# Performance work log

Hardware: AMD Instinct MI355X
Metric: run time of the kernel (lower is better)

The kernel has to match this reference:

```python
import jax, jax.numpy as jnp
import numpy as np

B, CIN, COUT, K, H, W = 8, 512, 512, 3, 64, 64
SCALE = 1.0 / np.sqrt(CIN * K * K).astype(np.float32)  # conv.scale
LRELU_SCALE = 1.4142135623730951  # sqrt(2), FusedLeakyReLU scale


def setup_inputs() -> dict:
    key = jax.random.key(0)
    ks = jax.random.split(key, 6)
    return {
        "x": jax.random.normal(ks[0], (B, CIN, H, W), jnp.float32),
        "style": jax.random.normal(ks[1], (B, CIN), jnp.float32),
        "noise": jax.random.normal(ks[2], (1, 1, H, W), jnp.float32),
        "weight": jax.random.normal(ks[3], (COUT, CIN, K, K), jnp.float32),
        "bias": jnp.zeros((COUT,), jnp.float32),
        "noise_strength": jax.random.uniform(ks[4], (1,), jnp.float32),
    }


def reference(x, style, noise, weight, bias, noise_strength):
    # Modulate: scale * weight * style  -> [B, Cout, Cin, K, K]
    w = SCALE * weight[None] * style[:, None, :, None, None]
    # Demodulate per (batch, out_channel)
    demod = jax.lax.rsqrt(jnp.sum(w * w, axis=(2, 3, 4)) + 1e-8)
    w = w * demod[:, :, None, None, None]
    # Per-sample conv (grouped-conv trick in torch) via vmap over batch
    pad = K // 2
    def conv_one(xi, wi):  # xi: [Cin,H,W], wi: [Cout,Cin,K,K]
        return jax.lax.conv_general_dilated(
            xi[None], wi, window_strides=(1, 1),
            padding=[(pad, pad), (pad, pad)],
            dimension_numbers=("NCHW", "OIHW", "NCHW"))[0]
    out = jax.vmap(conv_one)(x, w)  # [B, Cout, H, W]
    # NoiseInjection: out + strength * noise (noise broadcast over B, C)
    out = out + noise_strength[0] * noise
    # FusedLeakyReLU: leaky_relu(out + bias, 0.2) * sqrt(2)
    y = out + bias[None, :, None, None]
    return jnp.where(y >= 0, y, 0.2 * y) * LRELU_SCALE
```

## Files before the change

kernel.cpp:

```cpp
#include <hip/hip_runtime.h>
#include <hip/hip_bf16.h>

typedef __attribute__((ext_vector_type(8))) short s16x8;
typedef __attribute__((ext_vector_type(4))) float f32x4;

#define MOD_SCALE 0.014731391274719739f

__device__ __forceinline__ void gload_lds16(const void* g, void* l) {
    __builtin_amdgcn_global_load_lds(
        (const __attribute__((address_space(1))) unsigned int*)g,
        (__attribute__((address_space(3))) unsigned int*)l, 16, 0, 0);
}

__global__ __launch_bounds__(256) void k_border(__hip_bfloat16* __restrict__ xs) {
    const int idx = blockIdx.x * 256 + threadIdx.x;
    const int b = idx / 16640;
    const int r2 = idx - b * 16640;
    const int pair = r2 >> 6;
    const int ciq = r2 & 63;
    int pr, pc;
    if (pair < 66)       { pr = 0;          pc = pair; }
    else if (pair < 132) { pr = 65;         pc = pair - 66; }
    else if (pair < 196) { pr = pair - 131; pc = 0; }
    else                 { pr = pair - 195; pc = 65; }
    uint4* d = (uint4*)(xs + (((size_t)b * 66 + pr) * 66 + pc) * 512) + ciq;
    *d = make_uint4(0u, 0u, 0u, 0u);
}

__global__ __launch_bounds__(256) void k_xprep(const float* __restrict__ x,
                                               const float* __restrict__ style,
                                               __hip_bfloat16* __restrict__ xs) {
    const int cig = blockIdx.x, h = blockIdx.y, b = blockIdx.z;
    const int ci0 = cig * 128;
    __shared__ __align__(16) __hip_bfloat16 tile[64][130];
    const int t = threadIdx.x;
    const int wl = t & 63, cl4 = t >> 6;
    for (int r = 0; r < 32; ++r) {
        int c = r * 4 + cl4;
        float v = x[(((size_t)b * 512 + ci0 + c) * 64 + h) * 64 + wl];
        float s = style[b * 512 + ci0 + c];
        tile[wl][c] = __float2bfloat16(v * s * MOD_SCALE);
    }
    __syncthreads();
    const int w4 = t >> 6;
    const int cp = (t & 63) * 2;
    for (int r = 0; r < 16; ++r) {
        int w = r * 4 + w4;
        unsigned v = *(const unsigned*)(&tile[w][cp]);
        *(unsigned*)(&xs[(((size_t)b * 66 + h + 1) * 66 + (w + 1)) * 512 +
                         ci0 + cp]) = v;
    }
}

__global__ __launch_bounds__(256) void k_wprep(const float* __restrict__ w,
                                               __hip_bfloat16* __restrict__ wb) {
    __shared__ float lds[2304];
    const int t = threadIdx.x;
    const int p0 = blockIdx.x * 256;
    const float* src = w + (size_t)p0 * 9;
#pragma unroll
    for (int k = 0; k < 9; ++k) lds[k * 256 + t] = src[k * 256 + t];
    __syncthreads();
#pragma unroll
    for (int tap = 0; tap < 9; ++tap)
        wb[(size_t)tap * 262144 + p0 + t] = __float2bfloat16(lds[t * 9 + tap]);
}

__global__ __launch_bounds__(256) void k_demod(const float* __restrict__ w,
                                               const float* __restrict__ style,
                                               float* __restrict__ dem) {
    const int co = blockIdx.x;
    const int t = threadIdx.x;
    float accb[8] = {0.f, 0.f, 0.f, 0.f, 0.f, 0.f, 0.f, 0.f};
    for (int ci = t; ci < 512; ci += 256) {
        const float* wp = w + ((size_t)co * 512 + ci) * 9;
        float ws = 0.f;
#pragma unroll
        for (int k = 0; k < 9; ++k) { float v = wp[k]; ws += v * v; }
#pragma unroll
        for (int bb = 0; bb < 8; ++bb) {
            float s = style[bb * 512 + ci];
            accb[bb] += s * s * ws;
        }
    }
    __shared__ float red[256];
    const float S2 = MOD_SCALE * MOD_SCALE;
    for (int bb = 0; bb < 8; ++bb) {
        red[t] = accb[bb];
        __syncthreads();
        for (int off = 128; off > 0; off >>= 1) {
            if (t < off) red[t] += red[t + off];
            __syncthreads();
        }
        if (t == 0) dem[bb * 512 + co] = rsqrtf(S2 * red[0] + 1e-8f);
        __syncthreads();
    }
}

__global__ __launch_bounds__(256, 3) void k_conv(
    const __hip_bfloat16* __restrict__ xs,
    const __hip_bfloat16* __restrict__ wb,
    const float* __restrict__ demod,
    const float* __restrict__ noise,
    const float* __restrict__ bias,
    const float* __restrict__ nstr,
    float* __restrict__ out) {
    __shared__ __align__(16) char Xl[264 * 64];
    __shared__ __align__(16) char Wl[384 * 64];

    const int t = threadIdx.x;
    const int bi = blockIdx.x;
    const int co0 = (bi & 3) * 128;
    const int h0 = ((bi >> 2) & 31) * 2;
    const int b = bi >> 7;
    const int lane = t & 63;
    const int wv = t >> 6;
    const int wm = wv & 1, wn = wv >> 1;
    const int q = lane >> 4, ln = lane & 15;

    f32x4 acc[4][4];
#pragma unroll
    for (int i = 0; i < 4; ++i)
#pragma unroll
        for (int j = 0; j < 4; ++j) acc[i][j] = (f32x4){0.f, 0.f, 0.f, 0.f};

    const char* xsb = (const char*)xs + (size_t)b * 66 * 66 * 1024;
    const char* xsrc[4];
#pragma unroll
    for (int i = 0; i < 4; ++i) {
        int g = i * 256 + t;
        int e = g >> 2, s = g & 3;
        int r = e / 66, c = e - r * 66;
        int gc = s ^ (e & 3);
        xsrc[i] = xsb + (size_t)((h0 + r) * 66 + c) * 1024 + gc * 16;
    }
    const char* xsrct = xsb;
    {
        int e = 256 + (t >> 2), s = t & 3;
        int c = e - 198;
        int gc = s ^ (e & 3);
        xsrct = xsb + (size_t)((h0 + 3) * 66 + c) * 1024 + gc * 16;
    }
    const char* wsrc[6];
#pragma unroll
    for (int i = 0; i < 6; ++i) {
        int g = i * 256 + t;
        int e = g >> 2, s = g & 3;
        int rr = e >> 7, co = e & 127;
        int gc = s ^ (co & 3);
        wsrc[i] = (const char*)wb +
                  ((size_t)rr * 262144 + (size_t)(co0 + co) * 512) * 2 + gc * 16;
    }
    char* ldsXw = Xl + (wv << 10);
    char* ldsWw = Wl + (wv << 10);

    for (int cb = 0; cb < 16; ++cb) {
        const int cboff = cb * 64;
        __syncthreads();
#pragma unroll
        for (int i = 0; i < 4; ++i)
            gload_lds16(xsrc[i] + cboff, ldsXw + i * 4096);
        if (t < 32) gload_lds16(xsrct + cboff, Xl + 16384);
#pragma unroll
        for (int i = 0; i < 6; ++i)
            gload_lds16(wsrc[i] + cboff, ldsWw + i * 4096);
        __syncthreads();

        for (int dh = 0; dh < 3; ++dh) {
            if (dh) {
                __syncthreads();
#pragma unroll
                for (int i = 0; i < 6; ++i)
                    gload_lds16(wsrc[i] + dh * 1572864 + cboff, ldsWw + i * 4096);
                __syncthreads();
            }
            const int xrow = dh + wn;
#pragma unroll
            for (int dw = 0; dw < 3; ++dw) {
                s16x8 af[4], bfr[4];
                const char* abase =
                    Wl + (dw * 128 + wm * 64 + ln) * 64 + ((q ^ (ln & 3)) << 4);
#pragma unroll
                for (int mi = 0; mi < 4; ++mi)
                    af[mi] = *(const s16x8*)(abase + mi * 1024);
                const int ecol = xrow * 66 + dw + ln;
                const char* bbase = Xl + ecol * 64 + ((q ^ (ecol & 3)) << 4);
#pragma unroll
                for (int ni = 0; ni < 4; ++ni)
                    bfr[ni] = *(const s16x8*)(bbase + ni * 1024);
#pragma unroll
                for (int mi = 0; mi < 4; ++mi)
#pragma unroll
                    for (int ni = 0; ni < 4; ++ni)
                        acc[mi][ni] = __builtin_amdgcn_mfma_f32_16x16x32_bf16(
                            af[mi], bfr[ni], acc[mi][ni], 0, 0, 0);
            }
        }
    }

    const float nsv = nstr[0];
    const int h = h0 + wn;
    const float LR = 1.4142135623730951f;
#pragma unroll
    for (int mi = 0; mi < 4; ++mi) {
        float dm[4], bs[4];
#pragma unroll
        for (int r = 0; r < 4; ++r) {
            int co = co0 + wm * 64 + mi * 16 + q * 4 + r;
            dm[r] = demod[b * 512 + co];
            bs[r] = bias[co];
        }
#pragma unroll
        for (int ni = 0; ni < 4; ++ni) {
            int w = ni * 16 + ln;
            float nz = nsv * noise[h * 64 + w];
#pragma unroll
            for (int r = 0; r < 4; ++r) {
                int co = co0 + wm * 64 + mi * 16 + q * 4 + r;
                float v = acc[mi][ni][r] * dm[r] + nz + bs[r];
                v = (v >= 0.f ? v : 0.2f * v) * LR;
                out[(((size_t)b * 512 + co) * 64 + h) * 64 + w] = v;
            }
        }
    }
}

extern "C" void kernel_launch(void* const* d_in, const int* in_sizes, int n_in,
                              void* d_out, int out_size, void* d_ws, size_t ws_size,
                              hipStream_t stream) {
    const float* x      = (const float*)d_in[0];
    const float* style  = (const float*)d_in[1];
    const float* noise  = (const float*)d_in[2];
    const float* weight = (const float*)d_in[3];
    const float* bias   = (const float*)d_in[4];
    const float* nstr   = (const float*)d_in[5];
    float* out = (float*)d_out;

    char* ws = (char*)d_ws;
    __hip_bfloat16* xs = (__hip_bfloat16*)ws;
    __hip_bfloat16* wb = (__hip_bfloat16*)(ws + 35684352);
    float* demod = (float*)(ws + 35684352 + 4718592);

    k_border<<<520, 256, 0, stream>>>(xs);
    k_xprep<<<dim3(4, 64, 8), 256, 0, stream>>>(x, style, xs);
    k_wprep<<<1024, 256, 0, stream>>>(weight, wb);
    k_demod<<<512, 256, 0, stream>>>(weight, style, demod);
    k_conv<<<1024, 256, 0, stream>>>(xs, wb, demod, noise, bias, nstr, out);
}
```

Measured before the change: 289.0 us.

## Merge prep kernels and double-buffer per-tap weight tiles in conv

Folds the border-zero, input-modulation, weight-transpose and demodulation kernels into a single launch dispatched by block index, and rewrites the demod reduction to use wave shuffles with style squares staged in shared memory. The conv kernel now streams one tap's 128x64 weight tile at a time into a double buffer, prefetching the next tap while the current one computes. This shrinks LDS use enough to raise occupancy to 4 blocks per CU. The block mapping is also reordered so that adjacent blocks share output channels. The risks are one barrier per tap and more, smaller weight loads, while the input tile still reloads without overlap.

New measurement: 270.0 us. 1.07x faster.

```diff
diff --git a/kernel.cpp b/kernel.cpp
--- a/kernel.cpp
+++ b/kernel.cpp
@@ -12,92 +12,100 @@
         (__attribute__((address_space(3))) unsigned int*)l, 16, 0, 0);
 }
 
-__global__ __launch_bounds__(256) void k_border(__hip_bfloat16* __restrict__ xs) {
-    const int idx = blockIdx.x * 256 + threadIdx.x;
-    const int b = idx / 16640;
-    const int r2 = idx - b * 16640;
-    const int pair = r2 >> 6;
-    const int ciq = r2 & 63;
-    int pr, pc;
-    if (pair < 66)       { pr = 0;          pc = pair; }
-    else if (pair < 132) { pr = 65;         pc = pair - 66; }
-    else if (pair < 196) { pr = pair - 131; pc = 0; }
-    else                 { pr = pair - 195; pc = 65; }
-    uint4* d = (uint4*)(xs + (((size_t)b * 66 + pr) * 66 + pc) * 512) + ciq;
-    *d = make_uint4(0u, 0u, 0u, 0u);
-}
-
-__global__ __launch_bounds__(256) void k_xprep(const float* __restrict__ x,
-                                               const float* __restrict__ style,
-                                               __hip_bfloat16* __restrict__ xs) {
-    const int cig = blockIdx.x, h = blockIdx.y, b = blockIdx.z;
-    const int ci0 = cig * 128;
-    __shared__ __align__(16) __hip_bfloat16 tile[64][130];
+__global__ __launch_bounds__(256) void k_prep(const float* __restrict__ x,
+                                              const float* __restrict__ style,
+                                              const float* __restrict__ weight,
+                                              __hip_bfloat16* __restrict__ xs,
+                                              __hip_bfloat16* __restrict__ wb,
+                                              float* __restrict__ dem) {
+    __shared__ __align__(16) char sm[16896];
     const int t = threadIdx.x;
-    const int wl = t & 63, cl4 = t >> 6;
-    for (int r = 0; r < 32; ++r) {
-        int c = r * 4 + cl4;
-        float v = x[(((size_t)b * 512 + ci0 + c) * 64 + h) * 64 + wl];
-        float s = style[b * 512 + ci0 + c];
-        tile[wl][c] = __float2bfloat16(v * s * MOD_SCALE);
-    }
-    __syncthreads();
-    const int w4 = t >> 6;
-    const int cp = (t & 63) * 2;
-    for (int r = 0; r < 16; ++r) {
-        int w = r * 4 + w4;
-        unsigned v = *(const unsigned*)(&tile[w][cp]);
-        *(unsigned*)(&xs[(((size_t)b * 66 + h + 1) * 66 + (w + 1)) * 512 +
-                         ci0 + cp]) = v;
-    }
-}
-
-__global__ __launch_bounds__(256) void k_wprep(const float* __restrict__ w,
-                                               __hip_bfloat16* __restrict__ wb) {
-    __shared__ float lds[2304];
-    const int t = threadIdx.x;
-    const int p0 = blockIdx.x * 256;
-    const float* src = w + (size_t)p0 * 9;
-#pragma unroll
-    for (int k = 0; k < 9; ++k) lds[k * 256 + t] = src[k * 256 + t];
-    __syncthreads();
-#pragma unroll
-    for (int tap = 0; tap < 9; ++tap)
-        wb[(size_t)tap * 262144 + p0 + t] = __float2bfloat16(lds[t * 9 + tap]);
-}
-
-__global__ __launch_bounds__(256) void k_demod(const float* __restrict__ w,
-                                               const float* __restrict__ style,
-                                               float* __restrict__ dem) {
-    const int co = blockIdx.x;
-    const int t = threadIdx.x;
-    float accb[8] = {0.f, 0.f, 0.f, 0.f, 0.f, 0.f, 0.f, 0.f};
-    for (int ci = t; ci < 512; ci += 256) {
-        const float* wp = w + ((size_t)co * 512 + ci) * 9;
-        float ws = 0.f;
-#pragma unroll
-        for (int k = 0; k < 9; ++k) { float v = wp[k]; ws += v * v; }
-#pragma unroll
-        for (int bb = 0; bb < 8; ++bb) {
-            float s = style[bb * 512 + ci];
-            accb[bb] += s * s * ws;
-        }
-    }
-    __shared__ float red[256];
-    const float S2 = MOD_SCALE * MOD_SCALE;
-    for (int bb = 0; bb < 8; ++bb) {
-        red[t] = accb[bb];
-        __syncthreads();
-        for (int off = 128; off > 0; off >>= 1) {
-            if (t < off) red[t] += red[t + off];
-            __syncthreads();
-        }
-        if (t == 0) dem[bb * 512 + co] = rsqrtf(S2 * red[0] + 1e-8f);
-        __syncthreads();
-    }
-}
-
-__global__ __launch_bounds__(256, 3) void k_conv(
+    const int bid = blockIdx.x;
+
+    if (bid < 520) {
+        const int idx = bid * 256 + t;
+        const int b = idx / 16640;
+        const int r2 = idx - b * 16640;
+        const int pair = r2 >> 6;
+        const int ciq = r2 & 63;
+        int pr, pc;
+        if (pair < 66)       { pr = 0;          pc = pair; }
+        else if (pair < 132) { pr = 65;         pc = pair - 66; }
+        else if (pair < 196) { pr = pair - 131; pc = 0; }
+        else                 { pr = pair - 195; pc = 65; }
+        uint4* d = (uint4*)(xs + (((size_t)b * 66 + pr) * 66 + pc) * 512) + ciq;
+        *d = make_uint4(0u, 0u, 0u, 0u);
+    } else if (bid < 2568) {
+        const int r = bid - 520;
+        const int cig = r & 3, h = (r >> 2) & 63, b = r >> 8;
+        const int ci0 = cig * 128;
+        __hip_bfloat16 (*tile)[130] = (__hip_bfloat16(*)[130])sm;
+        const int wl = t & 63, cl4 = t >> 6;
+        for (int rr = 0; rr < 32; ++rr) {
+            int c = rr * 4 + cl4;
+            float v = x[(((size_t)b * 512 + ci0 + c) * 64 + h) * 64 + wl];
+            float s = style[b * 512 + ci0 + c];
+            tile[wl][c] = __float2bfloat16(v * s * MOD_SCALE);
+        }
+        __syncthreads();
+        const int w4 = t >> 6;
+        const int cp = (t & 63) * 2;
+        for (int rr = 0; rr < 16; ++rr) {
+            int w = rr * 4 + w4;
+            unsigned v = *(const unsigned*)(&tile[w][cp]);
+            *(unsigned*)(&xs[(((size_t)b * 66 + h + 1) * 66 + (w + 1)) * 512 +
+                             ci0 + cp]) = v;
+        }
+    } else if (bid < 3592) {
+        const int r = bid - 2568;
+        float* lds = (float*)sm;
+        const int p0 = r * 256;
+        const float* src = weight + (size_t)p0 * 9;
+#pragma unroll
+        for (int k = 0; k < 9; ++k) lds[k * 256 + t] = src[k * 256 + t];
+        __syncthreads();
+#pragma unroll
+        for (int tap = 0; tap < 9; ++tap)
+            wb[(size_t)tap * 262144 + p0 + t] = __float2bfloat16(lds[t * 9 + tap]);
+    } else {
+        const int co = bid - 3592;
+        float* s2 = (float*)sm;
+        for (int i = t; i < 4096; i += 256) { float v = style[i]; s2[i] = v * v; }
+        __syncthreads();
+        const float4* wp = (const float4*)(weight + (size_t)co * 4608);
+        float acc[8] = {0.f, 0.f, 0.f, 0.f, 0.f, 0.f, 0.f, 0.f};
+        for (int j = t; j < 1152; j += 256) {
+            float4 v = wp[j];
+            float w2[4] = {v.x * v.x, v.y * v.y, v.z * v.z, v.w * v.w};
+            int base = j * 4;
+#pragma unroll
+            for (int e = 0; e < 4; ++e) {
+                int ci = (base + e) / 9;
+                float ww = w2[e];
+#pragma unroll
+                for (int bb = 0; bb < 8; ++bb) acc[bb] += ww * s2[bb * 512 + ci];
+            }
+        }
+#pragma unroll
+        for (int bb = 0; bb < 8; ++bb)
+            for (int off = 32; off > 0; off >>= 1)
+                acc[bb] += __shfl_down(acc[bb], off);
+        float* red = (float*)(sm + 16384);
+        const int wv = t >> 6, lane = t & 63;
+        if (lane == 0) {
+#pragma unroll
+            for (int bb = 0; bb < 8; ++bb) red[wv * 8 + bb] = acc[bb];
+        }
+        __syncthreads();
+        if (t < 8) {
+            float s = red[t] + red[8 + t] + red[16 + t] + red[24 + t];
+            const float S2 = MOD_SCALE * MOD_SCALE;
+            dem[t * 512 + co] = rsqrtf(S2 * s + 1e-8f);
+        }
+    }
+}
+
+__global__ __launch_bounds__(256, 4) void k_conv(
     const __hip_bfloat16* __restrict__ xs,
     const __hip_bfloat16* __restrict__ wb,
     const float* __restrict__ demod,
@@ -105,14 +113,15 @@
     const float* __restrict__ bias,
     const float* __restrict__ nstr,
     float* __restrict__ out) {
-    __shared__ __align__(16) char Xl[264 * 64];
-    __shared__ __align__(16) char Wl[384 * 64];
+    __shared__ __align__(16) char Xl[16896];
+    __shared__ __align__(16) char Wl[2][8192];
 
     const int t = threadIdx.x;
     const int bi = blockIdx.x;
-    const int co0 = (bi & 3) * 128;
-    const int h0 = ((bi >> 2) & 31) * 2;
-    const int b = bi >> 7;
+    const int spat = bi & 255;
+    const int b = spat >> 5;
+    const int h0 = (spat & 31) << 1;
+    const int co0 = (bi >> 8) << 7;
     const int lane = t & 63;
     const int wv = t >> 6;
     const int wm = wv & 1, wn = wv >> 1;
@@ -134,67 +143,73 @@
         int gc = s ^ (e & 3);
         xsrc[i] = xsb + (size_t)((h0 + r) * 66 + c) * 1024 + gc * 16;
     }
-    const char* xsrct = xsb;
+    const char* xsrct;
     {
         int e = 256 + (t >> 2), s = t & 3;
         int c = e - 198;
         int gc = s ^ (e & 3);
         xsrct = xsb + (size_t)((h0 + 3) * 66 + c) * 1024 + gc * 16;
     }
-    const char* wsrc[6];
-#pragma unroll
-    for (int i = 0; i < 6; ++i) {
+    const char* wsrcb[2];
+#pragma unroll
+    for (int i = 0; i < 2; ++i) {
         int g = i * 256 + t;
         int e = g >> 2, s = g & 3;
-        int rr = e >> 7, co = e & 127;
-        int gc = s ^ (co & 3);
-        wsrc[i] = (const char*)wb +
-                  ((size_t)rr * 262144 + (size_t)(co0 + co) * 512) * 2 + gc * 16;
+        int gc = s ^ (e & 3);
+        wsrcb[i] = (const char*)wb + (size_t)(co0 + e) * 1024 + gc * 16;
     }
     char* ldsXw = Xl + (wv << 10);
-    char* ldsWw = Wl + (wv << 10);
-
+
+#pragma unroll
+    for (int i = 0; i < 4; ++i) gload_lds16(xsrc[i], ldsXw + i * 4096);
+    if (t < 32) gload_lds16(xsrct, Xl + 16384);
+#pragma unroll
+    for (int i = 0; i < 2; ++i)
+        gload_lds16(wsrcb[i], Wl[0] + (wv << 10) + i * 4096);
+    __syncthreads();
+
+    int g = 0;
     for (int cb = 0; cb < 16; ++cb) {
         const int cboff = cb * 64;
-        __syncthreads();
-#pragma unroll
-        for (int i = 0; i < 4; ++i)
-            gload_lds16(xsrc[i] + cboff, ldsXw + i * 4096);
-        if (t < 32) gload_lds16(xsrct + cboff, Xl + 16384);
-#pragma unroll
-        for (int i = 0; i < 6; ++i)
-            gload_lds16(wsrc[i] + cboff, ldsWw + i * 4096);
-        __syncthreads();
-
-        for (int dh = 0; dh < 3; ++dh) {
-            if (dh) {
-                __syncthreads();
-#pragma unroll
-                for (int i = 0; i < 6; ++i)
-                    gload_lds16(wsrc[i] + dh * 1572864 + cboff, ldsWw + i * 4096);
-                __syncthreads();
+#pragma unroll
+        for (int tap = 0; tap < 9; ++tap, ++g) {
+            if (tap < 8) {
+#pragma unroll
+                for (int i = 0; i < 2; ++i)
+                    gload_lds16(wsrcb[i] + (tap + 1) * 524288 + cboff,
+                                Wl[(g + 1) & 1] + (wv << 10) + i * 4096);
+            } else if (cb < 15) {
+#pragma unroll
+                for (int i = 0; i < 2; ++i)
+                    gload_lds16(wsrcb[i] + cboff + 64,
+                                Wl[(g + 1) & 1] + (wv << 10) + i * 4096);
             }
-            const int xrow = dh + wn;
-#pragma unroll
-            for (int dw = 0; dw < 3; ++dw) {
-                s16x8 af[4], bfr[4];
-                const char* abase =
-                    Wl + (dw * 128 + wm * 64 + ln) * 64 + ((q ^ (ln & 3)) << 4);
-#pragma unroll
-                for (int mi = 0; mi < 4; ++mi)
-                    af[mi] = *(const s16x8*)(abase + mi * 1024);
-                const int ecol = xrow * 66 + dw + ln;
-                const char* bbase = Xl + ecol * 64 + ((q ^ (ecol & 3)) << 4);
+            const int dh = tap / 3, dw = tap % 3;
+            const char* Wb = Wl[g & 1];
+            s16x8 af[4], bfr[4];
+            const char* abase = Wb + (wm * 64 + ln) * 64 + ((q ^ (ln & 3)) << 4);
+#pragma unroll
+            for (int mi = 0; mi < 4; ++mi)
+                af[mi] = *(const s16x8*)(abase + mi * 1024);
+            const int ecol = (dh + wn) * 66 + dw + ln;
+            const char* bbase = Xl + ecol * 64 + ((q ^ (ecol & 3)) << 4);
+#pragma unroll
+            for (int ni = 0; ni < 4; ++ni)
+                bfr[ni] = *(const s16x8*)(bbase + ni * 1024);
+#pragma unroll
+            for (int mi = 0; mi < 4; ++mi)
 #pragma unroll
                 for (int ni = 0; ni < 4; ++ni)
-                    bfr[ni] = *(const s16x8*)(bbase + ni * 1024);
-#pragma unroll
-                for (int mi = 0; mi < 4; ++mi)
-#pragma unroll
-                    for (int ni = 0; ni < 4; ++ni)
-                        acc[mi][ni] = __builtin_amdgcn_mfma_f32_16x16x32_bf16(
-                            af[mi], bfr[ni], acc[mi][ni], 0, 0, 0);
-            }
+                    acc[mi][ni] = __builtin_amdgcn_mfma_f32_16x16x32_bf16(
+                        af[mi], bfr[ni], acc[mi][ni], 0, 0, 0);
+            __syncthreads();
+        }
+        if (cb < 15) {
+#pragma unroll
+            for (int i = 0; i < 4; ++i)
+                gload_lds16(xsrc[i] + cboff + 64, ldsXw + i * 4096);
+            if (t < 32) gload_lds16(xsrct + cboff + 64, Xl + 16384);
+            __syncthreads();
         }
     }
 
@@ -241,9 +256,6 @@
     __hip_bfloat16* wb = (__hip_bfloat16*)(ws + 35684352);
     float* demod = (float*)(ws + 35684352 + 4718592);
 
-    k_border<<<520, 256, 0, stream>>>(xs);
-    k_xprep<<<dim3(4, 64, 8), 256, 0, stream>>>(x, style, xs);
-    k_wprep<<<1024, 256, 0, stream>>>(weight, wb);
-    k_demod<<<512, 256, 0, stream>>>(weight, style, demod);
+    k_prep<<<4104, 256, 0, stream>>>(x, style, weight, xs, wb, demod);
     k_conv<<<1024, 256, 0, stream>>>(xs, wb, demod, noise, bias, nstr, out);
 }
```
